# Performance work log

Measured on AMD Instinct MI355X. Metric: run time of the kernel, lower is better.

## Reference

```python
import jax, jax.numpy as jnp
import numpy as np

NEG_SLOPE = 0.01  # torch F.leaky_relu default

def leaky_relu(x):
    return jnp.where(x >= 0, x, NEG_SLOPE * x)

def setup_inputs() -> dict:
    key = jax.random.key(0)
    ks = jax.random.split(key, 16)
    N, D, H, L = 2048, 512, 256, 16
    # normalized-adjacency-like matrix: row sums ~0.5 to keep activations sane
    A_hat = jax.random.uniform(ks[0], (N, N), dtype=jnp.float32) / N
    X = jax.random.normal(ks[1], (N, D), dtype=jnp.float32)
    eps = jax.random.normal(ks[2], (N, L), dtype=jnp.float32)
    def lin(k, fan_out, fan_in):
        s = 1.0 / np.sqrt(fan_in)
        kw, kb = jax.random.split(k)
        W = jax.random.uniform(kw, (fan_out, fan_in), minval=-s, maxval=s, dtype=jnp.float32)
        b = jax.random.uniform(kb, (fan_out,), minval=-s, maxval=s, dtype=jnp.float32)
        return W, b
    W1, b1 = lin(ks[3], H, D)          # gcn1
    Wmu, bmu = lin(ks[4], L, H)        # gcn2_mu
    Wlv, blv = lin(ks[5], L, H)        # gcn2_logvar
    Wd1, bd1 = lin(ks[6], 2 * L, 2 * L)  # decoder_fc1
    Wd2, bd2 = lin(ks[7], 1, 2 * L)      # decoder_fc2
    return {"A_hat": A_hat, "X": X, "eps": eps,
            "W1": W1, "b1": b1, "Wmu": Wmu, "bmu": bmu,
            "Wlv": Wlv, "blv": blv, "Wd1": Wd1, "bd1": bd1,
            "Wd2": Wd2, "bd2": bd2}

def reference(A_hat, X, eps, W1, b1, Wmu, bmu, Wlv, blv, Wd1, bd1, Wd2, bd2):
    L = Wmu.shape[0]
    # --- encode: two GCN layers (A_hat @ X) @ W.T + b ---
    Hh = leaky_relu((A_hat @ X) @ W1.T + b1)           # [N, H]
    AH = A_hat @ Hh                                    # [N, H]
    mu = AH @ Wmu.T + bmu                              # [N, L]
    logvar = AH @ Wlv.T + blv                          # [N, L]
    # --- reparameterize ---
    Z = mu + eps * jnp.exp(0.5 * logvar)               # [N, L]
    # --- decode: pairwise MLP on concat(Z_i, Z_j), vectorized ---
    # fc1(concat(Zi,Zj)) = Zi @ Wd1[:, :L].T + Zj @ Wd1[:, L:].T + bd1
    P = Z @ Wd1[:, :L].T                               # [N, 2L]
    Q = Z @ Wd1[:, L:].T                               # [N, 2L]
    h = leaky_relu(P[:, None, :] + Q[None, :, :] + bd1)  # [N, N, 2L]
    A_pred = jax.nn.sigmoid(jnp.einsum('nmh,h->nm', h, Wd2[0]) + bd2[0])  # [N, N]
    return (A_pred, mu, logvar)
```

## Files before the change

### kernel.cpp

```cpp
#include <hip/hip_runtime.h>

#define NNODE 2048
#define DD    512
#define HHID  256
#define LLAT  16
#define H2    32

typedef __attribute__((ext_vector_type(8))) short  short8;
typedef __attribute__((ext_vector_type(4))) float  f32x4;

__device__ __forceinline__ unsigned short f2bf(float x) {
    unsigned int u = __float_as_uint(x);
    unsigned int r = (u + 0x7fffu + ((u >> 16) & 1u)) >> 16;
    return (unsigned short)r;
}
__device__ __forceinline__ float bf2f(unsigned short u) {
    return __uint_as_float(((unsigned int)u) << 16);
}

__global__ __launch_bounds__(256) void t0_cvt(const float* __restrict__ A,
                                              const float* __restrict__ X,
                                              const float* __restrict__ W1,
                                              unsigned short* __restrict__ Abf,
                                              unsigned short* __restrict__ Xbf,
                                              unsigned short* __restrict__ W1bf) {
    const int NT = 1343488;
    for (int v = blockIdx.x * 256 + threadIdx.x; v < NT; v += gridDim.x * 256) {
        const float* src; unsigned short* dst; int off;
        if (v < 1048576)      { src = A;  dst = Abf;  off = v; }
        else if (v < 1310720) { src = X;  dst = Xbf;  off = v - 1048576; }
        else                  { src = W1; dst = W1bf; off = v - 1310720; }
        float4 f = ((const float4*)src)[off];
        short4 h;
        h.x = (short)f2bf(f.x); h.y = (short)f2bf(f.y);
        h.z = (short)f2bf(f.z); h.w = (short)f2bf(f.w);
        ((short4*)dst)[off] = h;
    }
}

__global__ __launch_bounds__(256) void t1_mfma(const unsigned short* __restrict__ W1bf,
                                               const unsigned short* __restrict__ Xbf,
                                               float* __restrict__ XWp) {
    __shared__ __align__(16) unsigned short Ab[64][40];
    __shared__ __align__(16) unsigned short Bb[64][40];
    const int tid = threadIdx.x;
    const int n0 = blockIdx.x * 64;
    const int h0 = blockIdx.y * 64;
    const int ks = blockIdx.z;
    const int lane = tid & 63, wave = tid >> 6;
    const int wm = wave >> 1, wn = wave & 1;
    const int lm = lane & 15, lk = (lane >> 4) * 8;
    const int sr = tid >> 2, sc = (tid & 3) * 8;
    f32x4 acc[2][2] = {};
    for (int it = 0; it < 4; ++it) {
        int kk = ks * 128 + it * 32;
        *(uint4*)&Ab[sr][sc] = *(const uint4*)(W1bf + (size_t)(h0 + sr) * DD + kk + sc);
        *(uint4*)&Bb[sr][sc] = *(const uint4*)(Xbf  + (size_t)(n0 + sr) * DD + kk + sc);
        __syncthreads();
        short8 a0 = *(const short8*)&Ab[wm * 32 + lm][lk];
        short8 a1 = *(const short8*)&Ab[wm * 32 + 16 + lm][lk];
        short8 b0 = *(const short8*)&Bb[wn * 32 + lm][lk];
        short8 b1 = *(const short8*)&Bb[wn * 32 + 16 + lm][lk];
        acc[0][0] = __builtin_amdgcn_mfma_f32_16x16x32_bf16(a0, b0, acc[0][0], 0, 0, 0);
        acc[0][1] = __builtin_amdgcn_mfma_f32_16x16x32_bf16(a0, b1, acc[0][1], 0, 0, 0);
        acc[1][0] = __builtin_amdgcn_mfma_f32_16x16x32_bf16(a1, b0, acc[1][0], 0, 0, 0);
        acc[1][1] = __builtin_amdgcn_mfma_f32_16x16x32_bf16(a1, b1, acc[1][1], 0, 0, 0);
        __syncthreads();
    }
    float* outp = XWp + (size_t)ks * 524288;
    #pragma unroll
    for (int mi = 0; mi < 2; ++mi)
        #pragma unroll
        for (int ni = 0; ni < 2; ++ni)
            #pragma unroll
            for (int r = 0; r < 4; ++r) {
                int row = h0 + wm * 32 + mi * 16 + (lane >> 4) * 4 + r;
                int col = n0 + wn * 32 + ni * 16 + lm;
                outp[(size_t)row * NNODE + col] = acc[mi][ni][r];
            }
}

__global__ __launch_bounds__(256) void t1r(const float* __restrict__ XWp,
                                           unsigned short* __restrict__ XWt) {
    int v = blockIdx.x * 256 + threadIdx.x;
    const float4* p = (const float4*)XWp;
    float4 a = p[v];
    float4 b = p[v + 131072];
    float4 c = p[v + 262144];
    float4 d = p[v + 393216];
    float4 s;
    s.x = (a.x + b.x) + (c.x + d.x);
    s.y = (a.y + b.y) + (c.y + d.y);
    s.z = (a.z + b.z) + (c.z + d.z);
    s.w = (a.w + b.w) + (c.w + d.w);
    short4 h;
    h.x = (short)f2bf(s.x); h.y = (short)f2bf(s.y);
    h.z = (short)f2bf(s.z); h.w = (short)f2bf(s.w);
    ((short4*)XWt)[v] = h;
}

__global__ __launch_bounds__(256) void t2_mfma(const unsigned short* __restrict__ Abf,
                                               const unsigned short* __restrict__ XWt,
                                               float* __restrict__ Hp) {
    __shared__ __align__(16) unsigned short Ab[64][40];
    __shared__ __align__(16) unsigned short Bb[64][40];
    const int tid = threadIdx.x;
    const int m0 = blockIdx.x * 64;
    const int n0 = blockIdx.y * 64;
    const int ks = blockIdx.z;
    const int lane = tid & 63, wave = tid >> 6;
    const int wm = wave >> 1, wn = wave & 1;
    const int lm = lane & 15, lk = (lane >> 4) * 8;
    const int sr = tid >> 2, sc = (tid & 3) * 8;
    f32x4 acc[2][2] = {};
    for (int it = 0; it < 16; ++it) {
        int kk = ks * 512 + it * 32;
        *(uint4*)&Ab[sr][sc] = *(const uint4*)(Abf + (size_t)(m0 + sr) * NNODE + kk + sc);
        *(uint4*)&Bb[sr][sc] = *(const uint4*)(XWt + (size_t)(n0 + sr) * NNODE + kk + sc);
        __syncthreads();
        short8 a0 = *(const short8*)&Ab[wm * 32 + lm][lk];
        short8 a1 = *(const short8*)&Ab[wm * 32 + 16 + lm][lk];
        short8 b0 = *(const short8*)&Bb[wn * 32 + lm][lk];
        short8 b1 = *(const short8*)&Bb[wn * 32 + 16 + lm][lk];
        acc[0][0] = __builtin_amdgcn_mfma_f32_16x16x32_bf16(a0, b0, acc[0][0], 0, 0, 0);
        acc[0][1] = __builtin_amdgcn_mfma_f32_16x16x32_bf16(a0, b1, acc[0][1], 0, 0, 0);
        acc[1][0] = __builtin_amdgcn_mfma_f32_16x16x32_bf16(a1, b0, acc[1][0], 0, 0, 0);
        acc[1][1] = __builtin_amdgcn_mfma_f32_16x16x32_bf16(a1, b1, acc[1][1], 0, 0, 0);
        __syncthreads();
    }
    float* outp = Hp + (size_t)ks * 524288;
    #pragma unroll
    for (int mi = 0; mi < 2; ++mi)
        #pragma unroll
        for (int ni = 0; ni < 2; ++ni)
            #pragma unroll
            for (int r = 0; r < 4; ++r) {
                int row = m0 + wm * 32 + mi * 16 + (lane >> 4) * 4 + r;
                int col = n0 + wn * 32 + ni * 16 + lm;
                outp[(size_t)row * HHID + col] = acc[mi][ni][r];
            }
}

__global__ __launch_bounds__(256) void t2r(const float* __restrict__ Hp,
                                           const float* __restrict__ b1,
                                           unsigned short* __restrict__ Hbf) {
    int v = blockIdx.x * 256 + threadIdx.x;
    const float4* p = (const float4*)Hp;
    float4 a = p[v];
    float4 b = p[v + 131072];
    float4 c = p[v + 262144];
    float4 d = p[v + 393216];
    int dcol = (v & 63) * 4;
    float4 bb = *(const float4*)(b1 + dcol);
    float4 s;
    s.x = (a.x + b.x) + (c.x + d.x) + bb.x;
    s.y = (a.y + b.y) + (c.y + d.y) + bb.y;
    s.z = (a.z + b.z) + (c.z + d.z) + bb.z;
    s.w = (a.w + b.w) + (c.w + d.w) + bb.w;
    s.x = s.x >= 0.f ? s.x : 0.01f * s.x;
    s.y = s.y >= 0.f ? s.y : 0.01f * s.y;
    s.z = s.z >= 0.f ? s.z : 0.01f * s.z;
    s.w = s.w >= 0.f ? s.w : 0.01f * s.w;
    short4 h;
    h.x = (short)f2bf(s.x); h.y = (short)f2bf(s.y);
    h.z = (short)f2bf(s.z); h.w = (short)f2bf(s.w);
    ((short4*)Hbf)[v] = h;
}

__global__ __launch_bounds__(256) void t3_g(const unsigned short* __restrict__ Hbf,
                                            const float* __restrict__ Wmu,
                                            const float* __restrict__ Wlv,
                                            unsigned short* __restrict__ Gt) {
    __shared__ float Hs[8][260];
    __shared__ float Ws[32][260];
    const int tid = threadIdx.x;
    const int n0 = blockIdx.x * 8;
    #pragma unroll
    for (int s = 0; s < 8; ++s) {
        int idx = tid + s * 256;
        int row = idx >> 6, c = (idx & 63) * 4;
        const float* src = (row < 16) ? (Wmu + (size_t)row * HHID)
                                      : (Wlv + (size_t)(row - 16) * HHID);
        *(float4*)&Ws[row][c] = *(const float4*)(src + c);
    }
    {
        int r = tid >> 5, seg = tid & 31;
        int d = seg * 8;
        ushort4 u0 = *(const ushort4*)(Hbf + (size_t)(n0 + r) * HHID + d);
        ushort4 u1 = *(const ushort4*)(Hbf + (size_t)(n0 + r) * HHID + d + 4);
        Hs[r][d + 0] = bf2f(u0.x); Hs[r][d + 1] = bf2f(u0.y);
        Hs[r][d + 2] = bf2f(u0.z); Hs[r][d + 3] = bf2f(u0.w);
        Hs[r][d + 4] = bf2f(u1.x); Hs[r][d + 5] = bf2f(u1.y);
        Hs[r][d + 6] = bf2f(u1.z); Hs[r][d + 7] = bf2f(u1.w);
    }
    __syncthreads();
    const int r = tid >> 5, j = tid & 31;
    float acc = 0.f;
    #pragma unroll 8
    for (int d4 = 0; d4 < 64; ++d4) {
        float4 a = *(const float4*)&Hs[r][d4 * 4];
        float4 b = *(const float4*)&Ws[j][d4 * 4];
        acc += a.x * b.x + a.y * b.y + a.z * b.z + a.w * b.w;
    }
    Gt[(size_t)j * NNODE + n0 + r] = f2bf(acc);
}

__global__ __launch_bounds__(256) void t4_mfma(const unsigned short* __restrict__ Abf,
                                               const unsigned short* __restrict__ Gt,
                                               float* __restrict__ Mp) {
    __shared__ __align__(16) unsigned short Ab[64][40];
    __shared__ __align__(16) unsigned short Bb[32][40];
    const int tid = threadIdx.x;
    const int m0 = blockIdx.x * 64;
    const int ks = blockIdx.y;
    const int lane = tid & 63, wave = tid >> 6;
    const int lm = lane & 15, lk = (lane >> 4) * 8;
    const int sr = tid >> 2, sc = (tid & 3) * 8;
    f32x4 acc[2] = {};
    for (int it = 0; it < 8; ++it) {
        int kk = ks * 256 + it * 32;
        *(uint4*)&Ab[sr][sc] = *(const uint4*)(Abf + (size_t)(m0 + sr) * NNODE + kk + sc);
        if (tid < 128) {
            int row = tid >> 2, c = (tid & 3) * 8;
            *(uint4*)&Bb[row][c] = *(const uint4*)(Gt + (size_t)row * NNODE + kk + c);
        }
        __syncthreads();
        short8 a  = *(const short8*)&Ab[wave * 16 + lm][lk];
        short8 b0 = *(const short8*)&Bb[lm][lk];
        short8 b1 = *(const short8*)&Bb[16 + lm][lk];
        acc[0] = __builtin_amdgcn_mfma_f32_16x16x32_bf16(a, b0, acc[0], 0, 0, 0);
        acc[1] = __builtin_amdgcn_mfma_f32_16x16x32_bf16(a, b1, acc[1], 0, 0, 0);
        __syncthreads();
    }
    float* outp = Mp + (size_t)ks * 65536;
    #pragma unroll
    for (int ni = 0; ni < 2; ++ni)
        #pragma unroll
        for (int r = 0; r < 4; ++r) {
            int row = m0 + wave * 16 + (lane >> 4) * 4 + r;
            int col = ni * 16 + lm;
            outp[(size_t)row * H2 + col] = acc[ni][r];
        }
}

__global__ __launch_bounds__(256) void t5_z(const float* __restrict__ Mp,
                                            const float* __restrict__ bmu,
                                            const float* __restrict__ blv,
                                            const float* __restrict__ eps,
                                            const float* __restrict__ Wd1,
                                            const float* __restrict__ bd1,
                                            float* __restrict__ out_mu,
                                            float* __restrict__ out_lv,
                                            float* __restrict__ Pp,
                                            float* __restrict__ Qq) {
    __shared__ float Zs[16][16];
    const int tid = threadIdx.x;
    const int n0 = blockIdx.x * 16;
    {
        int nl = tid >> 4, l = tid & 15;
        int n = n0 + nl;
        float m = bmu[l], lv = blv[l];
        #pragma unroll
        for (int s = 0; s < 8; ++s) {
            m  += Mp[(size_t)s * 65536 + (size_t)n * H2 + l];
            lv += Mp[(size_t)s * 65536 + (size_t)n * H2 + 16 + l];
        }
        out_mu[(size_t)n * LLAT + l] = m;
        out_lv[(size_t)n * LLAT + l] = lv;
        Zs[nl][l] = m + eps[(size_t)n * LLAT + l] * __expf(0.5f * lv);
    }
    __syncthreads();
    #pragma unroll
    for (int p = 0; p < 2; ++p) {
        int idx = tid + p * 256;
        int nl = idx >> 5, o = idx & 31;
        int n = n0 + nl;
        float ap = bd1[o], aq = 0.f;
        #pragma unroll
        for (int l = 0; l < 16; ++l) {
            float z = Zs[nl][l];
            ap = fmaf(z, Wd1[o * H2 + l],      ap);
            aq = fmaf(z, Wd1[o * H2 + 16 + l], aq);
        }
        Pp[(size_t)n * H2 + o] = ap;
        Qq[(size_t)n * H2 + o] = aq;
    }
}

__global__ __launch_bounds__(256) void t6_dec(const float* __restrict__ Pp,
                                              const float* __restrict__ Qq,
                                              const float* __restrict__ Wd2,
                                              const float* __restrict__ bd2,
                                              float* __restrict__ Apred) {
    __shared__ float Qt[32][68];
    __shared__ float Ws2[32];
    const int tid = threadIdx.x;
    const int j0 = blockIdx.x * 64, i0 = blockIdx.y * 16;
    #pragma unroll
    for (int s = 0; s < 8; ++s) {
        int idx = tid + s * 256;
        int j = idx >> 5, o = idx & 31;
        Qt[o][j] = Qq[(size_t)(j0 + j) * H2 + o];
    }
    if (tid < 32) Ws2[tid] = Wd2[tid];
    const int i = i0 + (tid >> 4);
    const int jq = tid & 15;
    float p[32];
    const float4* P4 = (const float4*)(Pp + (size_t)i * H2);
    #pragma unroll
    for (int c = 0; c < 8; ++c) {
        float4 v = P4[c];
        p[c * 4] = v.x; p[c * 4 + 1] = v.y; p[c * 4 + 2] = v.z; p[c * 4 + 3] = v.w;
    }
    __syncthreads();
    f32x4 acc = {0.f, 0.f, 0.f, 0.f};
    #pragma unroll
    for (int o = 0; o < 32; ++o) {
        float4 q = *(const float4*)&Qt[o][jq * 4];
        float w = Ws2[o], po = p[o];
        float s0 = po + q.x, s1 = po + q.y, s2 = po + q.z, s3 = po + q.w;
        acc[0] = fmaf(w, fmaf(0.01f, fminf(s0, 0.f), fmaxf(s0, 0.f)), acc[0]);
        acc[1] = fmaf(w, fmaf(0.01f, fminf(s1, 0.f), fmaxf(s1, 0.f)), acc[1]);
        acc[2] = fmaf(w, fmaf(0.01f, fminf(s2, 0.f), fmaxf(s2, 0.f)), acc[2]);
        acc[3] = fmaf(w, fmaf(0.01f, fminf(s3, 0.f), fmaxf(s3, 0.f)), acc[3]);
    }
    float b = bd2[0];
    float4 r;
    r.x = 1.f / (1.f + __expf(-(acc[0] + b)));
    r.y = 1.f / (1.f + __expf(-(acc[1] + b)));
    r.z = 1.f / (1.f + __expf(-(acc[2] + b)));
    r.w = 1.f / (1.f + __expf(-(acc[3] + b)));
    *(float4*)(Apred + (size_t)i * NNODE + j0 + jq * 4) = r;
}

extern "C" void kernel_launch(void* const* d_in, const int* in_sizes, int n_in,
                              void* d_out, int out_size, void* d_ws, size_t ws_size,
                              hipStream_t stream) {
    const float* A   = (const float*)d_in[0];
    const float* X   = (const float*)d_in[1];
    const float* eps = (const float*)d_in[2];
    const float* W1  = (const float*)d_in[3];
    const float* b1  = (const float*)d_in[4];
    const float* Wmu = (const float*)d_in[5];
    const float* bmu = (const float*)d_in[6];
    const float* Wlv = (const float*)d_in[7];
    const float* blv = (const float*)d_in[8];
    const float* Wd1 = (const float*)d_in[9];
    const float* bd1 = (const float*)d_in[10];
    const float* Wd2 = (const float*)d_in[11];
    const float* bd2 = (const float*)d_in[12];
    float* out = (float*)d_out;
    char* ws = (char*)d_ws;

    unsigned short* Abf  = (unsigned short*)(ws);
    unsigned short* Xbf  = (unsigned short*)(ws + 8388608);
    unsigned short* W1bf = (unsigned short*)(ws + 10485760);
    float*          XWp  = (float*)(ws + 10747904);
    unsigned short* XWt  = (unsigned short*)(ws + 19136512);
    float*          Hp   = (float*)(ws + 20185088);
    unsigned short* Hbf  = (unsigned short*)(ws + 28573696);
    unsigned short* Gt   = (unsigned short*)(ws + 29622272);
    float*          Mp   = (float*)(ws + 29753344);
    float*          Pp   = (float*)(ws + 31850496);
    float*          Qq   = (float*)(ws + 32112640);

    float* out_mu = out + (size_t)NNODE * NNODE;
    float* out_lv = out_mu + NNODE * LLAT;

    t0_cvt <<<2048,            256, 0, stream>>>(A, X, W1, Abf, Xbf, W1bf);
    t1_mfma<<<dim3(32, 4, 4),  256, 0, stream>>>(W1bf, Xbf, XWp);
    t1r    <<<512,             256, 0, stream>>>(XWp, XWt);
    t2_mfma<<<dim3(32, 4, 4),  256, 0, stream>>>(Abf, XWt, Hp);
    t2r    <<<512,             256, 0, stream>>>(Hp, b1, Hbf);
    t3_g   <<<256,             256, 0, stream>>>(Hbf, Wmu, Wlv, Gt);
    t4_mfma<<<dim3(32, 8),     256, 0, stream>>>(Abf, Gt, Mp);
    t5_z   <<<128,             256, 0, stream>>>(Mp, bmu, blv, eps, Wd1, bd1,
                                                 out_mu, out_lv, Pp, Qq);
    t6_dec <<<dim3(32, 128),   256, 0, stream>>>(Pp, Qq, Wd2, bd2, out);
}
```

Before: 147.8 us.

## Drop split-K reduction kernels; use per-wave direct-load MFMA GEMMs with fused epilogues

Result: slower. 160.2 us (+8.4%).

```diff
diff --git a/kernel.cpp b/kernel.cpp
--- a/kernel.cpp
+++ b/kernel.cpp
@@ -40,131 +40,62 @@
 
 __global__ __launch_bounds__(256) void t1_mfma(const unsigned short* __restrict__ W1bf,
                                                const unsigned short* __restrict__ Xbf,
-                                               float* __restrict__ XWp) {
-    __shared__ __align__(16) unsigned short Ab[64][40];
-    __shared__ __align__(16) unsigned short Bb[64][40];
-    const int tid = threadIdx.x;
-    const int n0 = blockIdx.x * 64;
-    const int h0 = blockIdx.y * 64;
-    const int ks = blockIdx.z;
-    const int lane = tid & 63, wave = tid >> 6;
-    const int wm = wave >> 1, wn = wave & 1;
+                                               unsigned short* __restrict__ XWt) {
+    const int wt   = blockIdx.x * 4 + (threadIdx.x >> 6);
+    const int lane = threadIdx.x & 63;
+    const int h0 = (wt >> 7) * 16;
+    const int n0 = (wt & 127) * 16;
     const int lm = lane & 15, lk = (lane >> 4) * 8;
-    const int sr = tid >> 2, sc = (tid & 3) * 8;
-    f32x4 acc[2][2] = {};
-    for (int it = 0; it < 4; ++it) {
-        int kk = ks * 128 + it * 32;
-        *(uint4*)&Ab[sr][sc] = *(const uint4*)(W1bf + (size_t)(h0 + sr) * DD + kk + sc);
-        *(uint4*)&Bb[sr][sc] = *(const uint4*)(Xbf  + (size_t)(n0 + sr) * DD + kk + sc);
-        __syncthreads();
-        short8 a0 = *(const short8*)&Ab[wm * 32 + lm][lk];
-        short8 a1 = *(const short8*)&Ab[wm * 32 + 16 + lm][lk];
-        short8 b0 = *(const short8*)&Bb[wn * 32 + lm][lk];
-        short8 b1 = *(const short8*)&Bb[wn * 32 + 16 + lm][lk];
-        acc[0][0] = __builtin_amdgcn_mfma_f32_16x16x32_bf16(a0, b0, acc[0][0], 0, 0, 0);
-        acc[0][1] = __builtin_amdgcn_mfma_f32_16x16x32_bf16(a0, b1, acc[0][1], 0, 0, 0);
-        acc[1][0] = __builtin_amdgcn_mfma_f32_16x16x32_bf16(a1, b0, acc[1][0], 0, 0, 0);
-        acc[1][1] = __builtin_amdgcn_mfma_f32_16x16x32_bf16(a1, b1, acc[1][1], 0, 0, 0);
-        __syncthreads();
-    }
-    float* outp = XWp + (size_t)ks * 524288;
-    #pragma unroll
-    for (int mi = 0; mi < 2; ++mi)
-        #pragma unroll
-        for (int ni = 0; ni < 2; ++ni)
-            #pragma unroll
-            for (int r = 0; r < 4; ++r) {
-                int row = h0 + wm * 32 + mi * 16 + (lane >> 4) * 4 + r;
-                int col = n0 + wn * 32 + ni * 16 + lm;
-                outp[(size_t)row * NNODE + col] = acc[mi][ni][r];
-            }
-}
-
-__global__ __launch_bounds__(256) void t1r(const float* __restrict__ XWp,
-                                           unsigned short* __restrict__ XWt) {
-    int v = blockIdx.x * 256 + threadIdx.x;
-    const float4* p = (const float4*)XWp;
-    float4 a = p[v];
-    float4 b = p[v + 131072];
-    float4 c = p[v + 262144];
-    float4 d = p[v + 393216];
-    float4 s;
-    s.x = (a.x + b.x) + (c.x + d.x);
-    s.y = (a.y + b.y) + (c.y + d.y);
-    s.z = (a.z + b.z) + (c.z + d.z);
-    s.w = (a.w + b.w) + (c.w + d.w);
-    short4 h;
-    h.x = (short)f2bf(s.x); h.y = (short)f2bf(s.y);
-    h.z = (short)f2bf(s.z); h.w = (short)f2bf(s.w);
-    ((short4*)XWt)[v] = h;
+    const unsigned short* ap = W1bf + (size_t)(h0 + lm) * DD + lk;
+    const unsigned short* bp = Xbf  + (size_t)(n0 + lm) * DD + lk;
+    f32x4 acc = {};
+    #pragma unroll 4
+    for (int k = 0; k < DD; k += 32) {
+        short8 a = *(const short8*)(ap + k);
+        short8 b = *(const short8*)(bp + k);
+        acc = __builtin_amdgcn_mfma_f32_16x16x32_bf16(a, b, acc, 0, 0, 0);
+    }
+    const int col = n0 + lm;
+    #pragma unroll
+    for (int r = 0; r < 4; ++r) {
+        int row = h0 + (lane >> 4) * 4 + r;
+        XWt[(size_t)row * NNODE + col] = f2bf(acc[r]);
+    }
 }
 
 __global__ __launch_bounds__(256) void t2_mfma(const unsigned short* __restrict__ Abf,
                                                const unsigned short* __restrict__ XWt,
-                                               float* __restrict__ Hp) {
-    __shared__ __align__(16) unsigned short Ab[64][40];
-    __shared__ __align__(16) unsigned short Bb[64][40];
-    const int tid = threadIdx.x;
-    const int m0 = blockIdx.x * 64;
-    const int n0 = blockIdx.y * 64;
-    const int ks = blockIdx.z;
-    const int lane = tid & 63, wave = tid >> 6;
-    const int wm = wave >> 1, wn = wave & 1;
+                                               const float* __restrict__ bias1,
+                                               unsigned short* __restrict__ Hbf) {
+    const int wt   = blockIdx.x * 4 + (threadIdx.x >> 6);
+    const int lane = threadIdx.x & 63;
+    const int m0 = (wt >> 3) * 16;
+    const int n0 = (wt & 7) * 32;
     const int lm = lane & 15, lk = (lane >> 4) * 8;
-    const int sr = tid >> 2, sc = (tid & 3) * 8;
-    f32x4 acc[2][2] = {};
-    for (int it = 0; it < 16; ++it) {
-        int kk = ks * 512 + it * 32;
-        *(uint4*)&Ab[sr][sc] = *(const uint4*)(Abf + (size_t)(m0 + sr) * NNODE + kk + sc);
-        *(uint4*)&Bb[sr][sc] = *(const uint4*)(XWt + (size_t)(n0 + sr) * NNODE + kk + sc);
-        __syncthreads();
-        short8 a0 = *(const short8*)&Ab[wm * 32 + lm][lk];
-        short8 a1 = *(const short8*)&Ab[wm * 32 + 16 + lm][lk];
-        short8 b0 = *(const short8*)&Bb[wn * 32 + lm][lk];
-        short8 b1 = *(const short8*)&Bb[wn * 32 + 16 + lm][lk];
-        acc[0][0] = __builtin_amdgcn_mfma_f32_16x16x32_bf16(a0, b0, acc[0][0], 0, 0, 0);
-        acc[0][1] = __builtin_amdgcn_mfma_f32_16x16x32_bf16(a0, b1, acc[0][1], 0, 0, 0);
-        acc[1][0] = __builtin_amdgcn_mfma_f32_16x16x32_bf16(a1, b0, acc[1][0], 0, 0, 0);
-        acc[1][1] = __builtin_amdgcn_mfma_f32_16x16x32_bf16(a1, b1, acc[1][1], 0, 0, 0);
-        __syncthreads();
-    }
-    float* outp = Hp + (size_t)ks * 524288;
-    #pragma unroll
-    for (int mi = 0; mi < 2; ++mi)
-        #pragma unroll
-        for (int ni = 0; ni < 2; ++ni)
-            #pragma unroll
-            for (int r = 0; r < 4; ++r) {
-                int row = m0 + wm * 32 + mi * 16 + (lane >> 4) * 4 + r;
-                int col = n0 + wn * 32 + ni * 16 + lm;
-                outp[(size_t)row * HHID + col] = acc[mi][ni][r];
-            }
-}
-
-__global__ __launch_bounds__(256) void t2r(const float* __restrict__ Hp,
-                                           const float* __restrict__ b1,
-                                           unsigned short* __restrict__ Hbf) {
-    int v = blockIdx.x * 256 + threadIdx.x;
-    const float4* p = (const float4*)Hp;
-    float4 a = p[v];
-    float4 b = p[v + 131072];
-    float4 c = p[v + 262144];
-    float4 d = p[v + 393216];
-    int dcol = (v & 63) * 4;
-    float4 bb = *(const float4*)(b1 + dcol);
-    float4 s;
-    s.x = (a.x + b.x) + (c.x + d.x) + bb.x;
-    s.y = (a.y + b.y) + (c.y + d.y) + bb.y;
-    s.z = (a.z + b.z) + (c.z + d.z) + bb.z;
-    s.w = (a.w + b.w) + (c.w + d.w) + bb.w;
-    s.x = s.x >= 0.f ? s.x : 0.01f * s.x;
-    s.y = s.y >= 0.f ? s.y : 0.01f * s.y;
-    s.z = s.z >= 0.f ? s.z : 0.01f * s.z;
-    s.w = s.w >= 0.f ? s.w : 0.01f * s.w;
-    short4 h;
-    h.x = (short)f2bf(s.x); h.y = (short)f2bf(s.y);
-    h.z = (short)f2bf(s.z); h.w = (short)f2bf(s.w);
-    ((short4*)Hbf)[v] = h;
+    const unsigned short* ap  = Abf + (size_t)(m0 + lm) * NNODE + lk;
+    const unsigned short* bp0 = XWt + (size_t)(n0 + lm) * NNODE + lk;
+    const unsigned short* bp1 = XWt + (size_t)(n0 + 16 + lm) * NNODE + lk;
+    f32x4 acc0 = {}, acc1 = {};
+    #pragma unroll 4
+    for (int k = 0; k < NNODE; k += 32) {
+        short8 a  = *(const short8*)(ap + k);
+        short8 b0 = *(const short8*)(bp0 + k);
+        short8 b1 = *(const short8*)(bp1 + k);
+        acc0 = __builtin_amdgcn_mfma_f32_16x16x32_bf16(a, b0, acc0, 0, 0, 0);
+        acc1 = __builtin_amdgcn_mfma_f32_16x16x32_bf16(a, b1, acc1, 0, 0, 0);
+    }
+    const int col0 = n0 + lm, col1 = n0 + 16 + lm;
+    const float bv0 = bias1[col0], bv1 = bias1[col1];
+    #pragma unroll
+    for (int r = 0; r < 4; ++r) {
+        int row = m0 + (lane >> 4) * 4 + r;
+        float v0 = acc0[r] + bv0;
+        float v1 = acc1[r] + bv1;
+        v0 = fmaxf(v0, 0.01f * v0);
+        v1 = fmaxf(v1, 0.01f * v1);
+        Hbf[(size_t)row * HHID + col0] = f2bf(v0);
+        Hbf[(size_t)row * HHID + col1] = f2bf(v1);
+    }
 }
 
 __global__ __launch_bounds__(256) void t3_g(const unsigned short* __restrict__ Hbf,
@@ -208,39 +139,30 @@
 __global__ __launch_bounds__(256) void t4_mfma(const unsigned short* __restrict__ Abf,
                                                const unsigned short* __restrict__ Gt,
                                                float* __restrict__ Mp) {
-    __shared__ __align__(16) unsigned short Ab[64][40];
-    __shared__ __align__(16) unsigned short Bb[32][40];
-    const int tid = threadIdx.x;
-    const int m0 = blockIdx.x * 64;
-    const int ks = blockIdx.y;
-    const int lane = tid & 63, wave = tid >> 6;
+    const int wt   = blockIdx.x * 4 + (threadIdx.x >> 6);
+    const int lane = threadIdx.x & 63;
+    const int m0 = (wt >> 4) * 16;
+    const int nt = wt & 1;
+    const int ks = (wt >> 1) & 7;
+    const int n0 = nt * 16;
+    const int kbase = ks * 256;
     const int lm = lane & 15, lk = (lane >> 4) * 8;
-    const int sr = tid >> 2, sc = (tid & 3) * 8;
-    f32x4 acc[2] = {};
-    for (int it = 0; it < 8; ++it) {
-        int kk = ks * 256 + it * 32;
-        *(uint4*)&Ab[sr][sc] = *(const uint4*)(Abf + (size_t)(m0 + sr) * NNODE + kk + sc);
-        if (tid < 128) {
-            int row = tid >> 2, c = (tid & 3) * 8;
-            *(uint4*)&Bb[row][c] = *(const uint4*)(Gt + (size_t)row * NNODE + kk + c);
-        }
-        __syncthreads();
-        short8 a  = *(const short8*)&Ab[wave * 16 + lm][lk];
-        short8 b0 = *(const short8*)&Bb[lm][lk];
-        short8 b1 = *(const short8*)&Bb[16 + lm][lk];
-        acc[0] = __builtin_amdgcn_mfma_f32_16x16x32_bf16(a, b0, acc[0], 0, 0, 0);
-        acc[1] = __builtin_amdgcn_mfma_f32_16x16x32_bf16(a, b1, acc[1], 0, 0, 0);
-        __syncthreads();
+    const unsigned short* ap = Abf + (size_t)(m0 + lm) * NNODE + kbase + lk;
+    const unsigned short* bp = Gt  + (size_t)(n0 + lm) * NNODE + kbase + lk;
+    f32x4 acc = {};
+    #pragma unroll
+    for (int k = 0; k < 256; k += 32) {
+        short8 a = *(const short8*)(ap + k);
+        short8 b = *(const short8*)(bp + k);
+        acc = __builtin_amdgcn_mfma_f32_16x16x32_bf16(a, b, acc, 0, 0, 0);
     }
     float* outp = Mp + (size_t)ks * 65536;
-    #pragma unroll
-    for (int ni = 0; ni < 2; ++ni)
-        #pragma unroll
-        for (int r = 0; r < 4; ++r) {
-            int row = m0 + wave * 16 + (lane >> 4) * 4 + r;
-            int col = ni * 16 + lm;
-            outp[(size_t)row * H2 + col] = acc[ni][r];
-        }
+    const int col = n0 + lm;
+    #pragma unroll
+    for (int r = 0; r < 4; ++r) {
+        int row = m0 + (lane >> 4) * 4 + r;
+        outp[(size_t)row * H2 + col] = acc[r];
+    }
 }
 
 __global__ __launch_bounds__(256) void t5_z(const float* __restrict__ Mp,
@@ -319,10 +241,10 @@
         float4 q = *(const float4*)&Qt[o][jq * 4];
         float w = Ws2[o], po = p[o];
         float s0 = po + q.x, s1 = po + q.y, s2 = po + q.z, s3 = po + q.w;
-        acc[0] = fmaf(w, fmaf(0.01f, fminf(s0, 0.f), fmaxf(s0, 0.f)), acc[0]);
-        acc[1] = fmaf(w, fmaf(0.01f, fminf(s1, 0.f), fmaxf(s1, 0.f)), acc[1]);
-        acc[2] = fmaf(w, fmaf(0.01f, fminf(s2, 0.f), fmaxf(s2, 0.f)), acc[2]);
-        acc[3] = fmaf(w, fmaf(0.01f, fminf(s3, 0.f), fmaxf(s3, 0.f)), acc[3]);
+        acc[0] = fmaf(w, fmaxf(s0, 0.01f * s0), acc[0]);
+        acc[1] = fmaf(w, fmaxf(s1, 0.01f * s1), acc[1]);
+        acc[2] = fmaf(w, fmaxf(s2, 0.01f * s2), acc[2]);
+        acc[3] = fmaf(w, fmaxf(s3, 0.01f * s3), acc[3]);
     }
     float b = bd2[0];
     float4 r;
@@ -355,26 +277,22 @@
     unsigned short* Abf  = (unsigned short*)(ws);
     unsigned short* Xbf  = (unsigned short*)(ws + 8388608);
     unsigned short* W1bf = (unsigned short*)(ws + 10485760);
-    float*          XWp  = (float*)(ws + 10747904);
-    unsigned short* XWt  = (unsigned short*)(ws + 19136512);
-    float*          Hp   = (float*)(ws + 20185088);
-    unsigned short* Hbf  = (unsigned short*)(ws + 28573696);
-    unsigned short* Gt   = (unsigned short*)(ws + 29622272);
-    float*          Mp   = (float*)(ws + 29753344);
-    float*          Pp   = (float*)(ws + 31850496);
-    float*          Qq   = (float*)(ws + 32112640);
+    unsigned short* XWt  = (unsigned short*)(ws + 10747904);
+    unsigned short* Hbf  = (unsigned short*)(ws + 11796480);
+    unsigned short* Gt   = (unsigned short*)(ws + 12845056);
+    float*          Mp   = (float*)(ws + 12976128);
+    float*          Pp   = (float*)(ws + 15073280);
+    float*          Qq   = (float*)(ws + 15335424);
 
     float* out_mu = out + (size_t)NNODE * NNODE;
     float* out_lv = out_mu + NNODE * LLAT;
 
-    t0_cvt <<<2048,            256, 0, stream>>>(A, X, W1, Abf, Xbf, W1bf);
-    t1_mfma<<<dim3(32, 4, 4),  256, 0, stream>>>(W1bf, Xbf, XWp);
-    t1r    <<<512,             256, 0, stream>>>(XWp, XWt);
-    t2_mfma<<<dim3(32, 4, 4),  256, 0, stream>>>(Abf, XWt, Hp);
-    t2r    <<<512,             256, 0, stream>>>(Hp, b1, Hbf);
-    t3_g   <<<256,             256, 0, stream>>>(Hbf, Wmu, Wlv, Gt);
-    t4_mfma<<<dim3(32, 8),     256, 0, stream>>>(Abf, Gt, Mp);
-    t5_z   <<<128,             256, 0, stream>>>(Mp, bmu, blv, eps, Wd1, bd1,
-                                                 out_mu, out_lv, Pp, Qq);
-    t6_dec <<<dim3(32, 128),   256, 0, stream>>>(Pp, Qq, Wd2, bd2, out);
-}
+    t0_cvt <<<1024,          256, 0, stream>>>(A, X, W1, Abf, Xbf, W1bf);
+    t1_mfma<<<512,           256, 0, stream>>>(W1bf, Xbf, XWt);
+    t2_mfma<<<256,           256, 0, stream>>>(Abf, XWt, b1, Hbf);
+    t3_g   <<<256,           256, 0, stream>>>(Hbf, Wmu, Wlv, Gt);
+    t4_mfma<<<512,           256, 0, stream>>>(Abf, Gt, Mp);
+    t5_z   <<<128,           256, 0, stream>>>(Mp, bmu, blv, eps, Wd1, bd1,
+                                               out_mu, out_lv, Pp, Qq);
+    t6_dec <<<dim3(32, 128), 256, 0, stream>>>(Pp, Qq, Wd2, bd2, out);
+}
```
